# Performance work log

Hardware: AMD Instinct MI355X
Metric: run time of the kernel (lower is better)

Reference implementation:

```python
import jax, jax.numpy as jnp
import numpy as np

B, S, K, N = 8, 8192, 1024, 1024  # batch, seq, in_features, out_features

def setup_inputs() -> dict:
    key = jax.random.key(0)
    k1, k2, k3, k4 = jax.random.split(key, 4)
    x = jax.random.normal(k1, (B, S, K), dtype=jnp.float32)
    # int8 codes stored as float (matches fp16 CB parameter in the module)
    CB = jnp.clip(jnp.round(jax.random.normal(k2, (N, K), dtype=jnp.float32) * 42.0), -127.0, 127.0)
    # per-output-channel absmax scales (positive)
    SCB = jax.random.uniform(k3, (N,), dtype=jnp.float32, minval=0.5, maxval=2.0)
    bias = jax.random.normal(k4, (N,), dtype=jnp.float32) * 0.02
    return {"x": x, "CB": CB, "SCB": SCB, "bias": bias}

def reference(x, CB, SCB, bias):
    # out = linear(x, CB) * (SCB/127) + bias  -- scale applied AFTER the GEMM,
    # exactly as in the non-BFA forward path of my_8bit_linear.
    out = jnp.einsum('bsk,nk->bsn', x, CB)        # [B, S, N]
    out = out * (SCB * (1.0 / 127.0)) + bias      # per-output-channel dequant + bias
    return out
```

## Files before the change

kernel.cpp:

```cpp
#include <hip/hip_runtime.h>

typedef _Float16 half8 __attribute__((ext_vector_type(8)));
typedef _Float16 half4 __attribute__((ext_vector_type(4)));
typedef float    f32x4 __attribute__((ext_vector_type(4)));

constexpr int Mtot = 65536, Ntot = 1024, Ktot = 1024;
constexpr int BM = 256, BN = 256, BK = 64;
constexpr int KT = Ktot / BK;
constexpr int MT = Mtot / BM;
constexpr int NT = Ntot / BN;

constexpr size_t XH_BYTES  = (size_t)MT * KT * 2 * 1024 * 16;
constexpr size_t CBH_BYTES = (size_t)NT * KT * 2 * 1024 * 16;

__global__ __launch_bounds__(256)
void cvt_pack(const float* __restrict__ src, _Float16* __restrict__ dst)
{
    const int T = blockIdx.x * 256 + threadIdx.x;
    const float* s = src + (size_t)T * 8;
    f32x4 a = *(const f32x4*)s;
    f32x4 b = *(const f32x4*)(s + 4);
    half8 h = { (_Float16)a[0], (_Float16)a[1], (_Float16)a[2], (_Float16)a[3],
                (_Float16)b[0], (_Float16)b[1], (_Float16)b[2], (_Float16)b[3] };

    const int g    = T >> 7;
    const int k0   = (T & 127) << 3;
    const int tile = g >> 8;
    const int r    = g & 255;
    const int kt   = k0 >> 6;
    const int kh   = (k0 >> 5) & 1;
    const int hi   = (k0 >> 3) & 3;
    const int c    = r * 4 + (hi ^ ((r >> 1) & 3));
    *(half8*)(dst + (size_t)((tile * KT + kt) * 2 + kh) * 8192 + (size_t)c * 8) = h;
}

__global__ __launch_bounds__(512, 2)
void gemm8(const _Float16* __restrict__ Xh, const _Float16* __restrict__ CBh,
           const float* __restrict__ SCB,  const float* __restrict__ BIAS,
           float* __restrict__ OUT)
{
    __shared__ __align__(16) _Float16 lds[65536];

    const int nwg = gridDim.x;
    const int bid = blockIdx.x;
    const int wg  = (bid & 7) * (nwg >> 3) + (bid >> 3);
    const int nt  = wg & 3;
    const int mt  = wg >> 2;
    const int brow = mt * BM;
    const int bcol = nt * BN;

    const int tid  = threadIdx.x;
    const int lane = tid & 63;
    const int wid  = tid >> 6;
    const int wm   = wid >> 2;
    const int wn   = wid & 3;
    const int rA   = lane & 15;
    const int hi   = lane >> 4;
    const int sl   = hi ^ ((rA >> 1) & 3);

    const int aOff = (wm * 128 + rA) * 32 + sl * 8;
    const int bOff = (wn * 64  + rA) * 32 + sl * 8;

    f32x4 acc[8][4];
#pragma unroll
    for (int m = 0; m < 8; ++m)
#pragma unroll
        for (int n = 0; n < 4; ++n)
            acc[m][n] = (f32x4)0.0f;

    auto stageHalf = [&](int h) {
        const int kt = h >> 1, kh = h & 1, slot = h & 3;
        const _Float16* spA = Xh  + (size_t)((mt * KT + kt) * 2 + kh) * 8192;
        const _Float16* spB = CBh + (size_t)((nt * KT + kt) * 2 + kh) * 8192;
#pragma unroll
        for (int g = 0; g < 2; ++g) {
            const int cell = g * 512 + tid;
            __builtin_amdgcn_global_load_lds(
                (const __attribute__((address_space(1))) void*)(spA + (size_t)cell * 8),
                (__attribute__((address_space(3))) void*)(&lds[slot * 8192 + cell * 8]),
                16, 0, 0);
        }
#pragma unroll
        for (int g = 0; g < 2; ++g) {
            const int cell = g * 512 + tid;
            __builtin_amdgcn_global_load_lds(
                (const __attribute__((address_space(1))) void*)(spB + (size_t)cell * 8),
                (__attribute__((address_space(3))) void*)(&lds[32768 + slot * 8192 + cell * 8]),
                16, 0, 0);
        }
    };

    half8 bfk[4];
    auto phase = [&](int slot, int mh, bool loadB, auto&& stageFn, int vm) {
        half8 af[4];
        const int ab = slot * 8192;
#pragma unroll
        for (int f = 0; f < 4; ++f)
            af[f] = *(const half8*)&lds[ab + aOff + mh * 2048 + f * 512];
        if (loadB) {
#pragma unroll
            for (int n = 0; n < 4; ++n)
                bfk[n] = *(const half8*)&lds[32768 + ab + bOff + n * 512];
        }
        stageFn();
        __builtin_amdgcn_s_barrier();
        __builtin_amdgcn_s_setprio(1);
#pragma unroll
        for (int f = 0; f < 4; ++f)
#pragma unroll
            for (int n = 0; n < 4; ++n)
                acc[mh * 4 + f][n] = __builtin_amdgcn_mfma_f32_16x16x32_f16(
                    af[f], bfk[n], acc[mh * 4 + f][n], 0, 0, 0);
        __builtin_amdgcn_s_setprio(0);
        if (vm == 8)      asm volatile("s_waitcnt vmcnt(8)" ::: "memory");
        else if (vm == 4) asm volatile("s_waitcnt vmcnt(4)" ::: "memory");
        else if (vm == 0) asm volatile("s_waitcnt vmcnt(0)" ::: "memory");
        __builtin_amdgcn_s_barrier();
        __builtin_amdgcn_sched_barrier(0);
    };

    stageHalf(0); stageHalf(1); stageHalf(2);
    asm volatile("s_waitcnt vmcnt(8)" ::: "memory");
    __builtin_amdgcn_s_barrier();
    __builtin_amdgcn_sched_barrier(0);

    for (int t = 0; t < KT - 2; ++t) {
        const int s0 = (2 * t) & 3, s1 = (2 * t + 1) & 3;
        phase(s0, 0, true,  [&] { stageHalf(2 * t + 3); }, -1);
        phase(s0, 1, false, [] {},  8);
        phase(s1, 0, true,  [&] { stageHalf(2 * t + 4); }, -1);
        phase(s1, 1, false, [] {},  8);
    }
    phase(0, 0, true,  [&] { stageHalf(31); }, -1);
    phase(0, 1, false, [] {}, 8);
    phase(1, 0, true,  [] {}, -1);
    phase(1, 1, false, [] {}, 4);
    phase(2, 0, true,  [] {}, -1);
    phase(2, 1, false, [] {}, 0);
    phase(3, 0, true,  [] {}, -1);
    phase(3, 1, false, [] {}, -1);

    const float inv127 = 1.0f / 127.0f;
#pragma unroll
    for (int n = 0; n < 4; ++n) {
        const int col = bcol + wn * 64 + n * 16 + rA;
        const float s  = SCB[col] * inv127;
        const float bb = BIAS[col];
#pragma unroll
        for (int m = 0; m < 8; ++m) {
            const int grow = brow + wm * 128 + m * 16 + (hi << 2);
            float* op = OUT + (size_t)grow * Ntot + col;
#pragma unroll
            for (int j = 0; j < 4; ++j)
                op[(size_t)j * Ntot] = acc[m][n][j] * s + bb;
        }
    }
}

namespace fb {
constexpr int BMf = 128, BNf = 128, BKf = 32;
constexpr int KTf = Ktot / BKf;
constexpr int LDK = 40;

__global__ __launch_bounds__(256, 2)
void gemm_fb(const float* __restrict__ X, const float* __restrict__ CB,
             const float* __restrict__ SCB, const float* __restrict__ BIAS,
             float* __restrict__ OUT)
{
    __shared__ _Float16 As[2][BMf][LDK];
    __shared__ _Float16 Bs[2][BNf][LDK];

    const int nwg = gridDim.x;
    const int bid = blockIdx.x;
    const int wg  = (bid & 7) * (nwg >> 3) + (bid >> 3);
    const int ntile = wg & 7;
    const int mtile = wg >> 3;
    const int brow = mtile * BMf;
    const int bcol = ntile * BNf;

    const int tid = threadIdx.x, lane = tid & 63, wid = tid >> 6;
    const int wm = wid >> 1, wn = wid & 1;
    const int c4 = tid & 7, r0 = tid >> 3;
    const float* aBase = X  + (size_t)(brow + r0) * Ktot + c4 * 4;
    const float* bBase = CB + (size_t)(bcol + r0) * Ktot + c4 * 4;

    f32x4 acc[4][4];
#pragma unroll
    for (int m = 0; m < 4; ++m)
#pragma unroll
        for (int n = 0; n < 4; ++n) acc[m][n] = (f32x4)0.0f;

    float4 arg[4], brg[4];
    auto loadTiles = [&](int t) {
#pragma unroll
        for (int s = 0; s < 4; ++s) {
            arg[s] = *(const float4*)(aBase + (size_t)s * 32 * Ktot + t * BKf);
            brg[s] = *(const float4*)(bBase + (size_t)s * 32 * Ktot + t * BKf);
        }
    };
    auto writeTiles = [&](int buf) {
#pragma unroll
        for (int s = 0; s < 4; ++s) {
            const int row = r0 + s * 32;
            half4 ha = { (_Float16)arg[s].x, (_Float16)arg[s].y,
                         (_Float16)arg[s].z, (_Float16)arg[s].w };
            half4 hb = { (_Float16)brg[s].x, (_Float16)brg[s].y,
                         (_Float16)brg[s].z, (_Float16)brg[s].w };
            *(half4*)&As[buf][row][c4 * 4] = ha;
            *(half4*)&Bs[buf][row][c4 * 4] = hb;
        }
    };

    loadTiles(0); writeTiles(0); loadTiles(1);
    __syncthreads();
    const int rA = lane & 15, ko = (lane >> 4) * 8;

    for (int t = 0; t < KTf; ++t) {
        const int cur = t & 1;
        if (t + 1 < KTf) writeTiles(cur ^ 1);
        if (t + 2 < KTf) loadTiles(t + 2);
        half8 af[4], bf[4];
#pragma unroll
        for (int m = 0; m < 4; ++m) af[m] = *(const half8*)&As[cur][wm * 64 + m * 16 + rA][ko];
#pragma unroll
        for (int n = 0; n < 4; ++n) bf[n] = *(const half8*)&Bs[cur][wn * 64 + n * 16 + rA][ko];
#pragma unroll
        for (int m = 0; m < 4; ++m)
#pragma unroll
            for (int n = 0; n < 4; ++n)
                acc[m][n] = __builtin_amdgcn_mfma_f32_16x16x32_f16(af[m], bf[n], acc[m][n], 0, 0, 0);
        __syncthreads();
    }

    const float inv127 = 1.0f / 127.0f;
#pragma unroll
    for (int n = 0; n < 4; ++n) {
        const int col = bcol + wn * 64 + n * 16 + rA;
        const float s = SCB[col] * inv127;
        const float bb = BIAS[col];
#pragma unroll
        for (int m = 0; m < 4; ++m) {
            const int grow = brow + wm * 64 + m * 16 + ((lane >> 4) << 2);
            float* op = OUT + (size_t)grow * Ntot + col;
#pragma unroll
            for (int j = 0; j < 4; ++j) op[(size_t)j * Ntot] = acc[m][n][j] * s + bb;
        }
    }
}
}

extern "C" void kernel_launch(void* const* d_in, const int* in_sizes, int n_in,
                              void* d_out, int out_size, void* d_ws, size_t ws_size,
                              hipStream_t stream) {
    const float* X    = (const float*)d_in[0];
    const float* CB   = (const float*)d_in[1];
    const float* SCB  = (const float*)d_in[2];
    const float* BIAS = (const float*)d_in[3];
    float* OUT = (float*)d_out;

    if (ws_size < XH_BYTES + CBH_BYTES) {
        fb::gemm_fb<<<dim3(4096), dim3(256), 0, stream>>>(X, CB, SCB, BIAS, OUT);
        return;
    }

    _Float16* Xh  = (_Float16*)d_ws;
    _Float16* CBh = (_Float16*)((char*)d_ws + XH_BYTES);

    cvt_pack<<<dim3(32768), dim3(256), 0, stream>>>(X, Xh);
    cvt_pack<<<dim3(512),   dim3(256), 0, stream>>>(CB, CBh);
    gemm8<<<dim3(MT * NT), dim3(512), 0, stream>>>(Xh, CBh, SCB, BIAS, OUT);
}
```

Measured before the change: 584.1 us.

## Software-pipeline LDS fragment reads with double-buffered registers ahead of MFMAs

Restructures the main loop so A and B fragments for the next phase are read from LDS into alternate register sets while the current MFMA block runs, instead of loading and then immediately computing. It also halves the number of barriers per phase and simplifies global-to-LDS address computation using precomputed base pointers. This aims to hide LDS read latency behind matrix-core work. It increases register pressure, which is a concern under the 2-waves-per-SIMD launch bound, and reordered barriers must still keep slot reuse safe.

```diff
diff --git a/kernel.cpp b/kernel.cpp
--- a/kernel.cpp
+++ b/kernel.cpp
@@ -34,6 +34,33 @@
     *(half8*)(dst + (size_t)((tile * KT + kt) * 2 + kh) * 8192 + (size_t)c * 8) = h;
 }
 
+#define VMC(N) asm volatile("s_waitcnt vmcnt(" #N ")" ::: "memory")
+#define BAR()  __builtin_amdgcn_s_barrier()
+
+#define PREF_A(DST, slot, mh)                                              \
+    {   const int _ab = (slot) * 8192 + aOff + (mh) * 2048;                \
+        DST[0] = *(const half8*)&lds[_ab + 0 * 512];                       \
+        DST[1] = *(const half8*)&lds[_ab + 1 * 512];                       \
+        DST[2] = *(const half8*)&lds[_ab + 2 * 512];                       \
+        DST[3] = *(const half8*)&lds[_ab + 3 * 512]; }
+
+#define PREF_B(DST, slot)                                                  \
+    {   const int _bb = 32768 + (slot) * 8192 + bOff;                      \
+        DST[0] = *(const half8*)&lds[_bb + 0 * 512];                       \
+        DST[1] = *(const half8*)&lds[_bb + 1 * 512];                       \
+        DST[2] = *(const half8*)&lds[_bb + 2 * 512];                       \
+        DST[3] = *(const half8*)&lds[_bb + 3 * 512]; }
+
+#define MFMA16(AF, BF, MH)                                                 \
+    __builtin_amdgcn_s_setprio(1);                                         \
+    _Pragma("unroll")                                                      \
+    for (int f = 0; f < 4; ++f)                                            \
+        _Pragma("unroll")                                                  \
+        for (int n = 0; n < 4; ++n)                                        \
+            acc[(MH) * 4 + f][n] = __builtin_amdgcn_mfma_f32_16x16x32_f16( \
+                AF[f], BF[n], acc[(MH) * 4 + f][n], 0, 0, 0);              \
+    __builtin_amdgcn_s_setprio(0);
+
 __global__ __launch_bounds__(512, 2)
 void gemm8(const _Float16* __restrict__ Xh, const _Float16* __restrict__ CBh,
            const float* __restrict__ SCB,  const float* __restrict__ BIAS,
@@ -68,77 +95,59 @@
         for (int n = 0; n < 4; ++n)
             acc[m][n] = (f32x4)0.0f;
 
+    const _Float16* pAg = Xh  + (size_t)(mt * KT * 2) * 8192 + tid * 8;
+    const _Float16* pBg = CBh + (size_t)(nt * KT * 2) * 8192 + tid * 8;
+
     auto stageHalf = [&](int h) {
-        const int kt = h >> 1, kh = h & 1, slot = h & 3;
-        const _Float16* spA = Xh  + (size_t)((mt * KT + kt) * 2 + kh) * 8192;
-        const _Float16* spB = CBh + (size_t)((nt * KT + kt) * 2 + kh) * 8192;
-#pragma unroll
-        for (int g = 0; g < 2; ++g) {
-            const int cell = g * 512 + tid;
-            __builtin_amdgcn_global_load_lds(
-                (const __attribute__((address_space(1))) void*)(spA + (size_t)cell * 8),
-                (__attribute__((address_space(3))) void*)(&lds[slot * 8192 + cell * 8]),
-                16, 0, 0);
-        }
-#pragma unroll
-        for (int g = 0; g < 2; ++g) {
-            const int cell = g * 512 + tid;
-            __builtin_amdgcn_global_load_lds(
-                (const __attribute__((address_space(1))) void*)(spB + (size_t)cell * 8),
-                (__attribute__((address_space(3))) void*)(&lds[32768 + slot * 8192 + cell * 8]),
-                16, 0, 0);
-        }
+        const int slot = h & 3;
+        const _Float16* sA = pAg + (size_t)h * 8192;
+        const _Float16* sB = pBg + (size_t)h * 8192;
+        __builtin_amdgcn_global_load_lds(
+            (const __attribute__((address_space(1))) void*)sA,
+            (__attribute__((address_space(3))) void*)(&lds[slot * 8192 + tid * 8]), 16, 0, 0);
+        __builtin_amdgcn_global_load_lds(
+            (const __attribute__((address_space(1))) void*)(sA + 4096),
+            (__attribute__((address_space(3))) void*)(&lds[slot * 8192 + 4096 + tid * 8]), 16, 0, 0);
+        __builtin_amdgcn_global_load_lds(
+            (const __attribute__((address_space(1))) void*)sB,
+            (__attribute__((address_space(3))) void*)(&lds[32768 + slot * 8192 + tid * 8]), 16, 0, 0);
+        __builtin_amdgcn_global_load_lds(
+            (const __attribute__((address_space(1))) void*)(sB + 4096),
+            (__attribute__((address_space(3))) void*)(&lds[32768 + slot * 8192 + 4096 + tid * 8]), 16, 0, 0);
     };
 
-    half8 bfk[4];
-    auto phase = [&](int slot, int mh, bool loadB, auto&& stageFn, int vm) {
-        half8 af[4];
-        const int ab = slot * 8192;
-#pragma unroll
-        for (int f = 0; f < 4; ++f)
-            af[f] = *(const half8*)&lds[ab + aOff + mh * 2048 + f * 512];
-        if (loadB) {
-#pragma unroll
-            for (int n = 0; n < 4; ++n)
-                bfk[n] = *(const half8*)&lds[32768 + ab + bOff + n * 512];
-        }
-        stageFn();
-        __builtin_amdgcn_s_barrier();
-        __builtin_amdgcn_s_setprio(1);
-#pragma unroll
-        for (int f = 0; f < 4; ++f)
-#pragma unroll
-            for (int n = 0; n < 4; ++n)
-                acc[mh * 4 + f][n] = __builtin_amdgcn_mfma_f32_16x16x32_f16(
-                    af[f], bfk[n], acc[mh * 4 + f][n], 0, 0, 0);
-        __builtin_amdgcn_s_setprio(0);
-        if (vm == 8)      asm volatile("s_waitcnt vmcnt(8)" ::: "memory");
-        else if (vm == 4) asm volatile("s_waitcnt vmcnt(4)" ::: "memory");
-        else if (vm == 0) asm volatile("s_waitcnt vmcnt(0)" ::: "memory");
-        __builtin_amdgcn_s_barrier();
-        __builtin_amdgcn_sched_barrier(0);
-    };
+    half8 a0[4], a1[4], b0[4], b1[4];
 
     stageHalf(0); stageHalf(1); stageHalf(2);
-    asm volatile("s_waitcnt vmcnt(8)" ::: "memory");
-    __builtin_amdgcn_s_barrier();
-    __builtin_amdgcn_sched_barrier(0);
+    VMC(8);
+    BAR();
+    PREF_A(a0, 0, 0); PREF_B(b0, 0);
 
     for (int t = 0; t < KT - 2; ++t) {
-        const int s0 = (2 * t) & 3, s1 = (2 * t + 1) & 3;
-        phase(s0, 0, true,  [&] { stageHalf(2 * t + 3); }, -1);
-        phase(s0, 1, false, [] {},  8);
-        phase(s1, 0, true,  [&] { stageHalf(2 * t + 4); }, -1);
-        phase(s1, 1, false, [] {},  8);
-    }
-    phase(0, 0, true,  [&] { stageHalf(31); }, -1);
-    phase(0, 1, false, [] {}, 8);
-    phase(1, 0, true,  [] {}, -1);
-    phase(1, 1, false, [] {}, 4);
-    phase(2, 0, true,  [] {}, -1);
-    phase(2, 1, false, [] {}, 0);
-    phase(3, 0, true,  [] {}, -1);
-    phase(3, 1, false, [] {}, -1);
+        const int s0 = (2 * t) & 3, s1 = (2 * t + 1) & 3, s2 = (2 * t + 2) & 3;
+        PREF_A(a1, s0, 1);
+        stageHalf(2 * t + 3);
+        MFMA16(a0, b0, 0);
+        VMC(8); BAR();
+        PREF_A(a0, s1, 0); PREF_B(b1, s1);
+        MFMA16(a1, b0, 1);
+        BAR();
+        PREF_A(a1, s1, 1);
+        stageHalf(2 * t + 4);
+        MFMA16(a0, b1, 0);
+        VMC(8); BAR();
+        PREF_A(a0, s2, 0); PREF_B(b0, s2);
+        MFMA16(a1, b1, 1);
+        BAR();
+    }
+    PREF_A(a1, 0, 1); stageHalf(31); MFMA16(a0, b0, 0); VMC(8); BAR();
+    PREF_A(a0, 1, 0); PREF_B(b1, 1); MFMA16(a1, b0, 1);         BAR();
+    PREF_A(a1, 1, 1);                MFMA16(a0, b1, 0); VMC(4); BAR();
+    PREF_A(a0, 2, 0); PREF_B(b0, 2); MFMA16(a1, b1, 1);         BAR();
+    PREF_A(a1, 2, 1);                MFMA16(a0, b0, 0); VMC(0); BAR();
+    PREF_A(a0, 3, 0); PREF_B(b1, 3); MFMA16(a1, b0, 1);         BAR();
+    PREF_A(a1, 3, 1);                MFMA16(a0, b1, 0);         BAR();
+    MFMA16(a1, b1, 1);
 
     const float inv127 = 1.0f / 127.0f;
 #pragma unroll
```

Result: no change. 578.1 us (-1.0%).
